# Kernel tuning notes

Measured on AMD Instinct MI355X. Metric: run time of the kernel, lower is better.

Reference implementation:

```python
import jax, jax.numpy as jnp
import numpy as np

B, IN, COND, HID, LAT, E = 8192, 512, 256, 1024, 128, 4
EPS = 1e-4  # RunningMeanStd epsilon

def leaky(x):
    return jax.nn.leaky_relu(x, 0.01)

def _norm(a, m, v):
    # RunningMeanStd.normalize: clip((a-mean)/sqrt(var+eps), -5, 5)
    return jnp.clip((a - m) / jnp.sqrt(v + EPS), -5.0, 5.0)

def setup_inputs() -> dict:
    key = jax.random.key(0)
    ks = iter(jax.random.split(key, 64))
    def rn(shape, scale=0.02):
        return jax.random.normal(next(ks), shape, dtype=jnp.float32) * scale
    z32 = lambda *s: jnp.zeros(s, jnp.float32)
    return {
        'x': rn((B, IN), 1.0), 'w': rn((B, COND), 1.0), 'eps': rn((B, LAT), 1.0),
        'rms_in_mean': z32(IN), 'rms_in_var': jnp.ones((IN,), jnp.float32),
        'rms_c_mean': z32(COND), 'rms_c_var': jnp.ones((COND,), jnp.float32),
        'enc_w0': rn((IN + COND, HID)), 'enc_b0': z32(HID),
        'enc_w1': rn((COND + HID, HID)), 'enc_b1': z32(HID),
        'enc_w2': rn((COND + HID, HID)), 'enc_b2': z32(HID),
        'enc_w3': rn((COND + HID, HID)), 'enc_b3': z32(HID),
        'mu_w': rn((HID, LAT)), 'mu_b': z32(LAT),
        'lv_w': rn((HID, LAT)), 'lv_b': z32(LAT),
        'g_w0': rn((LAT + COND, 64)), 'g_b0': z32(64),
        'g_w1': rn((64, 64)), 'g_b1': z32(64),
        'g_w2': rn((64, E)), 'g_b2': z32(E),
        'dec_w0': rn((E, LAT + COND, HID)), 'dec_b0': jnp.full((E, HID), 0.01, jnp.float32),
        'dec_w1': rn((E, LAT + COND + HID, HID)), 'dec_b1': jnp.full((E, HID), 0.01, jnp.float32),
        'dec_w2': rn((E, LAT + COND + HID, HID)), 'dec_b2': jnp.full((E, HID), 0.01, jnp.float32),
        'dec_w3': rn((E, LAT + COND + HID, HID)), 'dec_b3': jnp.full((E, HID), 0.01, jnp.float32),
        'dec_w4': rn((E, LAT + COND + HID, IN)), 'dec_b4': jnp.full((E, IN), 0.01, jnp.float32),
    }

def _forward(x, w, eps, rms_in_mean, rms_in_var, rms_c_mean, rms_c_var,
             enc_w0, enc_b0, enc_w1, enc_b1, enc_w2, enc_b2, enc_w3, enc_b3,
             mu_w, mu_b, lv_w, lv_b,
             g_w0, g_b0, g_w1, g_b1, g_w2, g_b2,
             dec_w0, dec_b0, dec_w1, dec_b1, dec_w2, dec_b2, dec_w3, dec_b3,
             dec_w4, dec_b4):
    xn = _norm(x, rms_in_mean, rms_in_var)
    wn = _norm(w, rms_c_mean, rms_c_var)
    wn = jnp.where(jnp.isnan(wn), 0.0, wn)
    # encoder: original encode() loop applies ONLY the Linear ops (LeakyReLUs skipped),
    # concatenating w before every Linear after the first
    h = jnp.concatenate([xn, wn], -1) @ enc_w0 + enc_b0
    for W, b in ((enc_w1, enc_b1), (enc_w2, enc_b2), (enc_w3, enc_b3)):
        h = jnp.concatenate([wn, h], -1) @ W + b
    mu = leaky(h) @ mu_w + mu_b
    log_var = jnp.clip(leaky(h) @ lv_w + lv_b, -5.0, 5.0)
    z = mu + eps * jnp.exp(0.5 * log_var)  # reparameterize
    # MixedDecoder: gate -> softmax coefficients over experts
    c = wn
    g = leaky(jnp.concatenate([z, c], -1) @ g_w0 + g_b0)
    g = leaky(g @ g_w1 + g_b1)
    coeff = jax.nn.softmax(g @ g_w2 + g_b2, axis=-1)  # [B, E]
    out = c
    layers = ((dec_w0, dec_b0, True), (dec_w1, dec_b1, True),
              (dec_w2, dec_b2, True), (dec_w3, dec_b3, True),
              (dec_w4, dec_b4, False))
    for i, (W, b, act) in enumerate(layers):
        inp = jnp.concatenate([z, out], -1) if i == 0 else jnp.concatenate([z, c, out], -1)
        # fused soft-MoE: sum_e coeff_e * (inp @ W_e) + coeff @ b_e
        he = jnp.einsum('bi,eio->beo', inp, W)          # [B, E, out_dim]
        o = jnp.einsum('beo,be->bo', he, coeff) + coeff @ b
        out = leaky(o) if act else o
    return z, out, mu, log_var

def reference(x, w, eps, rms_in_mean, rms_in_var, rms_c_mean, rms_c_var,
              enc_w0, enc_b0, enc_w1, enc_b1, enc_w2, enc_b2, enc_w3, enc_b3,
              mu_w, mu_b, lv_w, lv_b,
              g_w0, g_b0, g_w1, g_b1, g_w2, g_b2,
              dec_w0, dec_b0, dec_w1, dec_b1, dec_w2, dec_b2, dec_w3, dec_b3,
              dec_w4, dec_b4):
    return _forward(x, w, eps, rms_in_mean, rms_in_var, rms_c_mean, rms_c_var,
                    enc_w0, enc_b0, enc_w1, enc_b1, enc_w2, enc_b2, enc_w3, enc_b3,
                    mu_w, mu_b, lv_w, lv_b,
                    g_w0, g_b0, g_w1, g_b1, g_w2, g_b2,
                    dec_w0, dec_b0, dec_w1, dec_b1, dec_w2, dec_b2, dec_w3, dec_b3,
                    dec_w4, dec_b4)
```

## Files before the change

kernel.cpp:

```cpp
#include <hip/hip_runtime.h>

#define BATCH 8192

typedef __bf16 bf16x8 __attribute__((ext_vector_type(8)));
typedef float f32x4 __attribute__((ext_vector_type(4)));

__device__ __forceinline__ float leakyf(float x) { return x > 0.f ? x : 0.01f * x; }

__device__ __forceinline__ short f2bf(float f) {
    union { float f; unsigned u; } v; v.f = f;
    unsigned r = v.u + 0x7fffu + ((v.u >> 16) & 1u);
    return (short)(r >> 16);
}
__device__ __forceinline__ float bf2f(short s) {
    union { unsigned u; float f; } v; v.u = ((unsigned)(unsigned short)s) << 16;
    return v.f;
}

__global__ __launch_bounds__(256) void transconv_k(const float* __restrict__ in,
                                                   short* __restrict__ out,
                                                   int R, int C, int ldo) {
    __shared__ float t[32][33];
    const int r0 = blockIdx.y * 32, c0 = blockIdx.x * 32;
    const int tx = threadIdx.x, ty = threadIdx.y;
#pragma unroll
    for (int i = 0; i < 4; ++i)
        t[ty * 4 + i][tx] = in[(size_t)(r0 + ty * 4 + i) * C + c0 + tx];
    __syncthreads();
#pragma unroll
    for (int i = 0; i < 4; ++i)
        out[(size_t)(c0 + ty * 4 + i) * ldo + r0 + tx] = f2bf(t[tx][ty * 4 + i]);
}

__global__ __launch_bounds__(256) void transconv_moe_k(const float* __restrict__ in,
                                                       short* __restrict__ out, int C) {
    __shared__ float t[32][33];
    const int r0 = blockIdx.y * 32, c0 = blockIdx.x * 32;
    const int tx = threadIdx.x, ty = threadIdx.y;
#pragma unroll
    for (int i = 0; i < 4; ++i)
        t[ty * 4 + i][tx] = in[(size_t)(r0 + ty * 4 + i) * C + c0 + tx];
    __syncthreads();
    const int e = r0 / 1408, k = r0 - e * 1408;
    const int rp0 = (k < 384) ? (e * 384 + k) : (1536 + e * 1024 + (k - 384));
#pragma unroll
    for (int i = 0; i < 4; ++i)
        out[(size_t)(c0 + ty * 4 + i) * 5632 + rp0 + tx] = f2bf(t[tx][ty * 4 + i]);
}

template <int BM, int EPI>
__global__ __launch_bounds__(512) void mm_p3(
    const short* __restrict__ A, int lda,
    const short* __restrict__ Bt, int ldb,
    const float* __restrict__ bias, const float* __restrict__ coeff,
    short* __restrict__ Cb, float* __restrict__ Cf, int ldc, int N, int K) {
    constexpr int TSZA = BM * 64;
    constexpr int TSZB = 128 * 64;
    constexpr int RA = BM / 64;
    constexpr int WMR = BM / 4;
    constexpr int FM = WMR / 16;
    __shared__ short As[3 * TSZA];
    __shared__ short Bs[2 * TSZB];
    const int tid = threadIdx.x;
    const int wave = tid >> 6, lane = tid & 63;
    const int wm = wave >> 1, wq = wave & 1;

    int bx = blockIdx.x, by = blockIdx.y;
    {
        int nwg = gridDim.x * gridDim.y;
        if ((nwg & 7) == 0) {
            int flat = by * gridDim.x + bx;
            int nf = (flat & 7) * (nwg >> 3) + (flat >> 3);
            bx = nf % gridDim.x;
            by = nf / gridDim.x;
        }
    }
    const int m0 = by * BM, n0 = bx * 128;
    const int srow = lane >> 3;
    const int scolsw = ((lane & 7) ^ srow) << 3;
    const int l15 = lane & 15;
    const int khalf = (lane >> 4) << 3;

    auto stageA = [&](int kt, int buf) {
#pragma unroll
        for (int it = 0; it < RA; ++it) {
            int chunk = it * 8 + wave;
            int row = chunk * 8 + srow;
            const short* g = A + (size_t)(m0 + row) * lda + kt + scolsw;
            __builtin_amdgcn_global_load_lds(
                (const __attribute__((address_space(1))) void*)g,
                (__attribute__((address_space(3))) void*)(As + buf * TSZA + chunk * 512),
                16, 0, 0);
        }
    };
    auto stageB = [&](int kt, int buf) {
#pragma unroll
        for (int it = 0; it < 2; ++it) {
            int chunk = it * 8 + wave;
            int row = chunk * 8 + srow;
            const short* g = Bt + (size_t)(n0 + row) * ldb + kt + scolsw;
            __builtin_amdgcn_global_load_lds(
                (const __attribute__((address_space(1))) void*)g,
                (__attribute__((address_space(3))) void*)(Bs + buf * TSZB + chunk * 512),
                16, 0, 0);
        }
    };

    f32x4 acc[FM][4];
    const f32x4 z4 = {0.f, 0.f, 0.f, 0.f};
#pragma unroll
    for (int i = 0; i < FM; ++i)
#pragma unroll
        for (int j = 0; j < 4; ++j) acc[i][j] = z4;

    auto loadA = [&](const short* Ah, int kk, bf16x8 (&a)[FM]) {
#pragma unroll
        for (int i = 0; i < FM; ++i) {
            int R = wm * WMR + i * 16 + l15;
            a[i] = *(const bf16x8*)&Ah[R * 64 + ((kk * 32 + khalf) ^ ((R & 7) << 3))];
        }
    };
    auto loadB = [&](const short* Bh, int kk, bf16x8 (&b)[4]) {
#pragma unroll
        for (int j = 0; j < 4; ++j) {
            int R = wq * 64 + j * 16 + l15;
            b[j] = *(const bf16x8*)&Bh[R * 64 + ((kk * 32 + khalf) ^ ((R & 7) << 3))];
        }
    };
    auto domfma = [&](bf16x8 (&a)[FM], bf16x8 (&b)[4]) {
        __builtin_amdgcn_s_setprio(1);
#pragma unroll
        for (int i = 0; i < FM; ++i)
#pragma unroll
            for (int j = 0; j < 4; ++j)
                acc[i][j] = __builtin_amdgcn_mfma_f32_16x16x32_bf16(
                    a[i], b[j], acc[i][j], 0, 0, 0);
        __builtin_amdgcn_s_setprio(0);
    };

    const int nk = K >> 6;

    stageA(0, 0);
    stageB(0, 0);
    stageA(64, 1);
    __builtin_amdgcn_sched_barrier(0);
    if constexpr (BM == 256) {
        asm volatile("s_waitcnt vmcnt(4)" ::: "memory");
    } else {
        asm volatile("s_waitcnt vmcnt(2)" ::: "memory");
    }
    __builtin_amdgcn_s_barrier();
    __builtin_amdgcn_sched_barrier(0);

    bf16x8 a0[FM], b0[4], a1[FM], b1[4];
    loadA(As, 0, a0);
    loadB(Bs, 0, b0);

    int ia = 0;
    int is = 2;
#pragma unroll 1
    for (int t = 0; t < nk; ++t) {
        const short* Ah = As + ia * TSZA;
        const short* Bh = Bs + (t & 1) * TSZB;
        const int ian = (ia == 2) ? 0 : ia + 1;
        const short* Ah1 = As + ian * TSZA;
        const short* Bh1 = Bs + ((t + 1) & 1) * TSZB;

        loadA(Ah, 1, a1);
        loadB(Bh, 1, b1);
        if (t + 1 < nk) stageB((t + 1) << 6, (t + 1) & 1);
        __builtin_amdgcn_sched_barrier(0);
        __builtin_amdgcn_s_barrier();
        __builtin_amdgcn_sched_barrier(0);
        domfma(a0, b0);
        __builtin_amdgcn_sched_barrier(0);
        asm volatile("s_waitcnt vmcnt(0)" ::: "memory");
        __builtin_amdgcn_s_barrier();
        __builtin_amdgcn_sched_barrier(0);

        if (t + 1 < nk) {
            loadA(Ah1, 0, a0);
            loadB(Bh1, 0, b0);
        }
        if (t + 2 < nk) stageA((t + 2) << 6, is);
        __builtin_amdgcn_sched_barrier(0);
        __builtin_amdgcn_s_barrier();
        __builtin_amdgcn_sched_barrier(0);
        domfma(a1, b1);
        __builtin_amdgcn_sched_barrier(0);

        ia = ian;
        is = (is == 2) ? 0 : is + 1;
    }

#pragma unroll
    for (int i = 0; i < FM; ++i) {
#pragma unroll
        for (int r = 0; r < 4; ++r) {
            int row = m0 + wm * WMR + i * 16 + ((lane >> 4) << 2) + r;
#pragma unroll
            for (int j = 0; j < 4; ++j) {
                int col = n0 + wq * 64 + j * 16 + l15;
                float v = acc[i][j][r];
                if constexpr (EPI == 0) {
                    v += bias[col];
                    Cb[(size_t)row * ldc + col] = f2bf(v);
                } else if constexpr (EPI == 1) {
                    v = leakyf(v + bias[col]);
                    Cb[(size_t)row * ldc + col] = f2bf(v);
                } else if constexpr (EPI == 5) {
                    const float4 c4 = *reinterpret_cast<const float4*>(coeff + (size_t)row * 4);
                    v += c4.x * bias[col] + c4.y * bias[N + col] +
                         c4.z * bias[2 * N + col] + c4.w * bias[3 * N + col];
                    float a = leakyf(v);
                    Cb[(size_t)row * ldc + 0 * 1024 + col] = f2bf(c4.x * a);
                    Cb[(size_t)row * ldc + 1 * 1024 + col] = f2bf(c4.y * a);
                    Cb[(size_t)row * ldc + 2 * 1024 + col] = f2bf(c4.z * a);
                    Cb[(size_t)row * ldc + 3 * 1024 + col] = f2bf(c4.w * a);
                } else {
                    const float4 c4 = *reinterpret_cast<const float4*>(coeff + (size_t)row * 4);
                    v += c4.x * bias[col] + c4.y * bias[N + col] +
                         c4.z * bias[2 * N + col] + c4.w * bias[3 * N + col];
                    Cf[(size_t)row * ldc + col] = v;
                }
            }
        }
    }
}

template <int BM, int BN, int EPI>
__global__ __launch_bounds__(256) void mm_k(
    const short* __restrict__ A, int lda,
    const short* __restrict__ Bt, int ldb,
    const float* __restrict__ bias, const float* __restrict__ bias2,
    const float* __restrict__ coeff,
    short* __restrict__ Cb, float* __restrict__ Cf, float* __restrict__ Cf2,
    int ldc, int N, int K) {
    constexpr bool MOE = (EPI == 3 || EPI == 4);
    constexpr int WM = BM / 2, WN = BN / 2;
    constexpr int FM = WM / 16, FN = WN / 16;
    constexpr int ASZ = BM * 64, BSZ = BN * 64;
    __shared__ short As[2 * ASZ];
    __shared__ short Bs[2 * BSZ];
    const int tid = threadIdx.x;
    const int wave = tid >> 6, lane = tid & 63;
    const int wm = wave >> 1, wq = wave & 1;

    int bx = blockIdx.x, by = blockIdx.y;
    {
        int nwg = gridDim.x * gridDim.y;
        if ((nwg & 7) == 0) {
            int flat = by * gridDim.x + bx;
            int nf = (flat & 7) * (nwg >> 3) + (flat >> 3);
            bx = nf % gridDim.x;
            by = nf / gridDim.x;
        }
    }
    const int m0 = by * BM, n0 = bx * BN;
    const int srow = lane >> 3;
    const int scolsw = ((lane & 7) ^ srow) << 3;
    const int l15 = lane & 15;
    const int khalf = (lane >> 4) << 3;

    auto stage = [&](const short* Bsrc, int kt, int half) {
#pragma unroll
        for (int it = 0; it < BM / 32; ++it) {
            int chunk = it * 4 + wave;
            int row = chunk * 8 + srow;
            const short* g = A + (size_t)(m0 + row) * lda + kt + scolsw;
            __builtin_amdgcn_global_load_lds(
                (const __attribute__((address_space(1))) void*)g,
                (__attribute__((address_space(3))) void*)(As + half * ASZ + chunk * 512),
                16, 0, 0);
        }
#pragma unroll
        for (int it = 0; it < BN / 32; ++it) {
            int chunk = it * 4 + wave;
            int row = chunk * 8 + srow;
            const short* g = Bsrc + (size_t)(n0 + row) * ldb + kt + scolsw;
            __builtin_amdgcn_global_load_lds(
                (const __attribute__((address_space(1))) void*)g,
                (__attribute__((address_space(3))) void*)(Bs + half * BSZ + chunk * 512),
                16, 0, 0);
        }
    };

    f32x4 acc[FM][FN];
    f32x4 accf[MOE ? FM : 1][MOE ? FN : 1];
    const f32x4 z4 = {0.f, 0.f, 0.f, 0.f};
    if constexpr (MOE) {
#pragma unroll
        for (int i = 0; i < FM; ++i)
#pragma unroll
            for (int j = 0; j < FN; ++j) accf[i][j] = z4;
    }

    constexpr int NE = MOE ? 4 : 1;
    const int nk = K >> 6;
#pragma unroll 1
    for (int e = 0; e < NE; ++e) {
        const short* Be = Bt + (size_t)e * K;
#pragma unroll
        for (int i = 0; i < FM; ++i)
#pragma unroll
            for (int j = 0; j < FN; ++j) acc[i][j] = z4;

        stage(Be, 0, 0);
        __syncthreads();

#pragma unroll 1
        for (int t = 0; t < nk; ++t) {
            const int cur = t & 1;
            if (t + 1 < nk) stage(Be, (t + 1) << 6, cur ^ 1);
            const short* Ah = As + cur * ASZ;
            const short* Bh = Bs + cur * BSZ;
#pragma unroll
            for (int kk = 0; kk < 2; ++kk) {
                bf16x8 a[FM], b[FN];
#pragma unroll
                for (int i = 0; i < FM; ++i) {
                    int R = wm * WM + i * 16 + l15;
                    int off = (kk * 32 + khalf) ^ ((R & 7) << 3);
                    a[i] = *(const bf16x8*)&Ah[R * 64 + off];
                }
#pragma unroll
                for (int j = 0; j < FN; ++j) {
                    int R = wq * WN + j * 16 + l15;
                    int off = (kk * 32 + khalf) ^ ((R & 7) << 3);
                    b[j] = *(const bf16x8*)&Bh[R * 64 + off];
                }
#pragma unroll
                for (int i = 0; i < FM; ++i)
#pragma unroll
                    for (int j = 0; j < FN; ++j)
                        acc[i][j] = __builtin_amdgcn_mfma_f32_16x16x32_bf16(
                            a[i], b[j], acc[i][j], 0, 0, 0);
            }
            __syncthreads();
        }
        if constexpr (MOE) {
#pragma unroll
            for (int i = 0; i < FM; ++i) {
                int rbase = m0 + wm * WM + i * 16 + ((lane >> 4) << 2);
#pragma unroll
                for (int r = 0; r < 4; ++r) {
                    float ce = coeff[(size_t)(rbase + r) * 4 + e];
#pragma unroll
                    for (int j = 0; j < FN; ++j) accf[i][j][r] += ce * acc[i][j][r];
                }
            }
        }
    }

#pragma unroll
    for (int i = 0; i < FM; ++i) {
#pragma unroll
        for (int r = 0; r < 4; ++r) {
            int row = m0 + wm * WM + i * 16 + ((lane >> 4) << 2) + r;
#pragma unroll
            for (int j = 0; j < FN; ++j) {
                int col = n0 + wq * WN + j * 16 + l15;
                float v = MOE ? accf[i][j][r] : acc[i][j][r];
                if constexpr (EPI == 0) {
                    v += bias[col];
                    Cb[(size_t)row * ldc + col] = f2bf(v);
                } else if constexpr (EPI == 1) {
                    v = leakyf(v + bias[col]);
                    Cb[(size_t)row * ldc + col] = f2bf(v);
                } else if constexpr (EPI == 2) {
                    if (col < 128) {
                        Cf[(size_t)row * 128 + col] = v + bias[col];
                    } else {
                        float u = v + bias2[col - 128];
                        u = fminf(fmaxf(u, -5.f), 5.f);
                        Cf2[(size_t)row * 128 + (col - 128)] = u;
                    }
                } else if constexpr (EPI == 3) {
                    const float* c4 = coeff + (size_t)row * 4;
                    v += c4[0] * bias[col] + c4[1] * bias[N + col] +
                         c4[2] * bias[2 * N + col] + c4[3] * bias[3 * N + col];
                    Cb[(size_t)row * ldc + col] = f2bf(leakyf(v));
                } else {
                    const float* c4 = coeff + (size_t)row * 4;
                    v += c4[0] * bias[col] + c4[1] * bias[N + col] +
                         c4[2] * bias[2 * N + col] + c4[3] * bias[3 * N + col];
                    Cf[(size_t)row * ldc + col] = v;
                }
            }
        }
    }
}

__global__ __launch_bounds__(256) void norm_k(
    const float* __restrict__ x, const float* __restrict__ w,
    const float* __restrict__ im, const float* __restrict__ iv,
    const float* __restrict__ cm, const float* __restrict__ cv,
    short* __restrict__ enc0, short* __restrict__ encA,
    short* __restrict__ encB, short* __restrict__ dec0) {
    int idx = blockIdx.x * 256 + threadIdx.x;
    const int TX = BATCH * 512;
    if (idx < TX) {
        int b = idx >> 9, j = idx & 511;
        float v = (x[idx] - im[j]) * rsqrtf(iv[j] + 1e-4f);
        v = fminf(fmaxf(v, -5.f), 5.f);
        enc0[(size_t)b * 768 + j] = f2bf(v);
    } else {
        int k = idx - TX;
        if (k < BATCH * 256) {
            int b = k >> 8, j = k & 255;
            float v = (w[k] - cm[j]) * rsqrtf(cv[j] + 1e-4f);
            if (v != v) v = 0.f;
            v = fminf(fmaxf(v, -5.f), 5.f);
            short s = f2bf(v);
            enc0[(size_t)b * 768 + 512 + j] = s;
            encA[(size_t)b * 1280 + j] = s;
            encB[(size_t)b * 1280 + j] = s;
            dec0[(size_t)b * 384 + 128 + j] = s;
        }
    }
}

__global__ __launch_bounds__(256) void reparam_k(
    const float* __restrict__ mu, const float* __restrict__ lv,
    const float* __restrict__ eps, float* __restrict__ z, short* __restrict__ dec0) {
    int idx = blockIdx.x * 256 + threadIdx.x;
    if (idx >= BATCH * 128) return;
    float zv = mu[idx] + eps[idx] * expf(0.5f * lv[idx]);
    z[idx] = zv;
    int b = idx >> 7, j = idx & 127;
    dec0[(size_t)b * 384 + j] = f2bf(zv);
}

__global__ __launch_bounds__(256) void fill_zc_k(const short* __restrict__ dec0,
                                                 const float* __restrict__ cf,
                                                 short* __restrict__ dA,
                                                 short* __restrict__ dB) {
    int idx = blockIdx.x * 256 + threadIdx.x;
    if (idx >= BATCH * 1536) return;
    int b = idx / 1536, c = idx - b * 1536;
    int e = c / 384, k = c - e * 384;
    short s = f2bf(cf[(size_t)b * 4 + e] * bf2f(dec0[(size_t)b * 384 + k]));
    dA[(size_t)b * 5632 + c] = s;
    dB[(size_t)b * 5632 + c] = s;
}

__global__ __launch_bounds__(256) void fill_dec_k(const short* __restrict__ dec0,
                                                  short* __restrict__ decA,
                                                  short* __restrict__ decB) {
    int idx = blockIdx.x * 256 + threadIdx.x;
    if (idx >= BATCH * 384) return;
    int b = idx / 384, c = idx - b * 384;
    short s = dec0[idx];
    decA[(size_t)b * 1408 + c] = s;
    decB[(size_t)b * 1408 + c] = s;
}

__global__ __launch_bounds__(256) void gate_sm_k(const short* __restrict__ g1,
                                                 const float* __restrict__ w2,
                                                 const float* __restrict__ b2,
                                                 float* __restrict__ coeff) {
    int r = blockIdx.x * 256 + threadIdx.x;
    if (r >= BATCH) return;
    float l0 = b2[0], l1 = b2[1], l2 = b2[2], l3 = b2[3];
    const short* row = g1 + (size_t)r * 64;
#pragma unroll
    for (int k = 0; k < 64; ++k) {
        float gv = bf2f(row[k]);
        l0 += gv * w2[k * 4 + 0];
        l1 += gv * w2[k * 4 + 1];
        l2 += gv * w2[k * 4 + 2];
        l3 += gv * w2[k * 4 + 3];
    }
    float mx = fmaxf(fmaxf(l0, l1), fmaxf(l2, l3));
    float e0 = expf(l0 - mx), e1 = expf(l1 - mx), e2 = expf(l2 - mx), e3 = expf(l3 - mx);
    float s = 1.f / (e0 + e1 + e2 + e3);
    float4 outv = make_float4(e0 * s, e1 * s, e2 * s, e3 * s);
    *reinterpret_cast<float4*>(coeff + (size_t)r * 4) = outv;
}

extern "C" void kernel_launch(void* const* d_in, const int* in_sizes, int n_in,
                              void* d_out, int out_size, void* d_ws, size_t ws_size,
                              hipStream_t stream) {
    const float* x    = (const float*)d_in[0];
    const float* w    = (const float*)d_in[1];
    const float* epsv = (const float*)d_in[2];
    const float* rim  = (const float*)d_in[3];
    const float* riv  = (const float*)d_in[4];
    const float* rcm  = (const float*)d_in[5];
    const float* rcv  = (const float*)d_in[6];
    const float* ew0 = (const float*)d_in[7];  const float* eb0 = (const float*)d_in[8];
    const float* ew1 = (const float*)d_in[9];  const float* eb1 = (const float*)d_in[10];
    const float* ew2 = (const float*)d_in[11]; const float* eb2 = (const float*)d_in[12];
    const float* ew3 = (const float*)d_in[13]; const float* eb3 = (const float*)d_in[14];
    const float* muw = (const float*)d_in[15]; const float* mub = (const float*)d_in[16];
    const float* lvw = (const float*)d_in[17]; const float* lvb = (const float*)d_in[18];
    const float* gw0 = (const float*)d_in[19]; const float* gb0 = (const float*)d_in[20];
    const float* gw1 = (const float*)d_in[21]; const float* gb1 = (const float*)d_in[22];
    const float* gw2 = (const float*)d_in[23]; const float* gb2 = (const float*)d_in[24];
    const float* dw0 = (const float*)d_in[25]; const float* db0 = (const float*)d_in[26];
    const float* dw1 = (const float*)d_in[27]; const float* db1 = (const float*)d_in[28];
    const float* dw2 = (const float*)d_in[29]; const float* db2 = (const float*)d_in[30];
    const float* dw3 = (const float*)d_in[31]; const float* db3 = (const float*)d_in[32];
    const float* dw4 = (const float*)d_in[33]; const float* db4 = (const float*)d_in[34];

    float* out    = (float*)d_out;
    float* z_out  = out;
    float* y_out  = out + (size_t)BATCH * 128;
    float* mu_out = out + (size_t)BATCH * 640;
    float* lv_out = out + (size_t)BATCH * 768;

    char* cur = (char*)d_ws;
    auto alloc = [&](size_t bytes) -> char* {
        char* p = cur;
        cur += (bytes + 255) & ~(size_t)255;
        return p;
    };
    auto align256 = [](size_t b) { return (b + 255) & ~(size_t)255; };

    short* ew0t = (short*)alloc((size_t)768 * 1024 * 2);
    short* ew1t = (short*)alloc((size_t)1280 * 1024 * 2);
    short* ew2t = (short*)alloc((size_t)1280 * 1024 * 2);
    short* ew3t = (short*)alloc((size_t)1280 * 1024 * 2);
    short* hdWt = (short*)alloc((size_t)256 * 1024 * 2);
    short* gw0t = (short*)alloc((size_t)64 * 384 * 2);
    short* gw1t = (short*)alloc((size_t)64 * 64 * 2);
    short* dw0t = (short*)alloc((size_t)1024 * 1536 * 2);
    short* dw1t = (short*)alloc((size_t)1024 * 5632 * 2);
    short* dw2t = (short*)alloc((size_t)1024 * 5632 * 2);
    short* dw3t = (short*)alloc((size_t)1024 * 5632 * 2);
    short* dw4t = (short*)alloc((size_t)512 * 5632 * 2);
    short* dec0 = (short*)alloc((size_t)BATCH * 384 * 2);
    short* g0   = (short*)alloc((size_t)BATCH * 64 * 2);
    short* g1   = (short*)alloc((size_t)BATCH * 64 * 2);
    float* cf   = (float*)alloc((size_t)BATCH * 4 * 4);

    char* region = cur;
    const size_t bigA = align256((size_t)BATCH * 5632 * 2);
    const size_t fastNeed = (size_t)(region - (char*)d_ws) + 2 * bigA;
    const bool fast = (ws_size >= fastNeed);

    short* enc0 = (short*)region;
    short* encA = (short*)(region + align256((size_t)BATCH * 768 * 2));
    short* encB = (short*)((char*)encA + align256((size_t)BATCH * 1280 * 2));
    short* hl   = encB;
    short* dAp = (short*)region;
    short* dBp = (short*)(region + bigA);
    short* decA = (short*)region;
    short* decB = (short*)(region + align256((size_t)BATCH * 1408 * 2));

    dim3 blk(256);
    dim3 blk5(512);
    dim3 tblk(32, 8);

    transconv_k<<<dim3(1024 / 32, 768 / 32), tblk, 0, stream>>>(ew0, ew0t, 768, 1024, 768);
    transconv_k<<<dim3(1024 / 32, 1280 / 32), tblk, 0, stream>>>(ew1, ew1t, 1280, 1024, 1280);
    transconv_k<<<dim3(1024 / 32, 1280 / 32), tblk, 0, stream>>>(ew2, ew2t, 1280, 1024, 1280);
    transconv_k<<<dim3(1024 / 32, 1280 / 32), tblk, 0, stream>>>(ew3, ew3t, 1280, 1024, 1280);
    transconv_k<<<dim3(128 / 32, 1024 / 32), tblk, 0, stream>>>(muw, hdWt, 1024, 128, 1024);
    transconv_k<<<dim3(128 / 32, 1024 / 32), tblk, 0, stream>>>(lvw, hdWt + (size_t)128 * 1024, 1024, 128, 1024);
    transconv_k<<<dim3(64 / 32, 384 / 32), tblk, 0, stream>>>(gw0, gw0t, 384, 64, 384);
    transconv_k<<<dim3(64 / 32, 64 / 32), tblk, 0, stream>>>(gw1, gw1t, 64, 64, 64);
    transconv_k<<<dim3(1024 / 32, 1536 / 32), tblk, 0, stream>>>(dw0, dw0t, 1536, 1024, 1536);
    if (fast) {
        transconv_moe_k<<<dim3(1024 / 32, 5632 / 32), tblk, 0, stream>>>(dw1, dw1t, 1024);
        transconv_moe_k<<<dim3(1024 / 32, 5632 / 32), tblk, 0, stream>>>(dw2, dw2t, 1024);
        transconv_moe_k<<<dim3(1024 / 32, 5632 / 32), tblk, 0, stream>>>(dw3, dw3t, 1024);
        transconv_moe_k<<<dim3(512 / 32, 5632 / 32), tblk, 0, stream>>>(dw4, dw4t, 512);
    } else {
        transconv_k<<<dim3(1024 / 32, 5632 / 32), tblk, 0, stream>>>(dw1, dw1t, 5632, 1024, 5632);
        transconv_k<<<dim3(1024 / 32, 5632 / 32), tblk, 0, stream>>>(dw2, dw2t, 5632, 1024, 5632);
        transconv_k<<<dim3(1024 / 32, 5632 / 32), tblk, 0, stream>>>(dw3, dw3t, 5632, 1024, 5632);
        transconv_k<<<dim3(512 / 32, 5632 / 32), tblk, 0, stream>>>(dw4, dw4t, 5632, 512, 5632);
    }

    norm_k<<<dim3(BATCH * 768 / 256), blk, 0, stream>>>(x, w, rim, riv, rcm, rcv,
                                                        enc0, encA, encB, dec0);

    dim3 gBig(1024 / 128, BATCH / 256);
    mm_p3<256, 0><<<gBig, blk5, 0, stream>>>(enc0, 768, ew0t, 768, eb0, nullptr,
                                             encA + 256, nullptr, 1280, 1024, 768);
    mm_p3<256, 0><<<gBig, blk5, 0, stream>>>(encA, 1280, ew1t, 1280, eb1, nullptr,
                                             encB + 256, nullptr, 1280, 1024, 1280);
    mm_p3<256, 0><<<gBig, blk5, 0, stream>>>(encB, 1280, ew2t, 1280, eb2, nullptr,
                                             encA + 256, nullptr, 1280, 1024, 1280);
    mm_p3<256, 1><<<gBig, blk5, 0, stream>>>(encA, 1280, ew3t, 1280, eb3, nullptr,
                                             hl, nullptr, 1024, 1024, 1280);

    mm_k<64, 128, 2><<<dim3(2, BATCH / 64), blk, 0, stream>>>(hl, 1024, hdWt, 1024, mub, lvb,
                                                              nullptr, nullptr, mu_out, lv_out,
                                                              0, 256, 1024);

    reparam_k<<<dim3(BATCH * 128 / 256), blk, 0, stream>>>(mu_out, lv_out, epsv, z_out, dec0);

    mm_k<64, 64, 1><<<dim3(1, BATCH / 64), blk, 0, stream>>>(dec0, 384, gw0t, 384, gb0, nullptr,
                                                             nullptr, g0, nullptr, nullptr,
                                                             64, 64, 384);
    mm_k<64, 64, 1><<<dim3(1, BATCH / 64), blk, 0, stream>>>(g0, 64, gw1t, 64, gb1, nullptr,
                                                             nullptr, g1, nullptr, nullptr,
                                                             64, 64, 64);
    gate_sm_k<<<dim3(BATCH / 256), blk, 0, stream>>>(g1, gw2, gb2, cf);

    if (fast) {
        fill_zc_k<<<dim3(BATCH * 1536 / 256), blk, 0, stream>>>(dec0, cf, dAp, dBp);
        mm_p3<256, 5><<<gBig, blk5, 0, stream>>>(dAp, 5632, dw0t, 1536, db0, cf,
                                                 dAp + 1536, nullptr, 5632, 1024, 1536);
        mm_p3<256, 5><<<gBig, blk5, 0, stream>>>(dAp, 5632, dw1t, 5632, db1, cf,
                                                 dBp + 1536, nullptr, 5632, 1024, 5632);
        mm_p3<256, 5><<<gBig, blk5, 0, stream>>>(dBp, 5632, dw2t, 5632, db2, cf,
                                                 dAp + 1536, nullptr, 5632, 1024, 5632);
        mm_p3<256, 5><<<gBig, blk5, 0, stream>>>(dAp, 5632, dw3t, 5632, db3, cf,
                                                 dBp + 1536, nullptr, 5632, 1024, 5632);
        mm_p3<128, 6><<<dim3(512 / 128, BATCH / 128), blk5, 0, stream>>>(
            dBp, 5632, dw4t, 5632, db4, cf, nullptr, y_out, 512, 512, 5632);
    } else {
        fill_dec_k<<<dim3(BATCH * 384 / 256), blk, 0, stream>>>(dec0, decA, decB);
        dim3 gDec(1024 / 128, BATCH / 128);
        mm_k<128, 128, 3><<<gDec, blk, 0, stream>>>(dec0, 384, dw0t, 1536, db0, nullptr, cf,
                                                    decA + 384, nullptr, nullptr, 1408, 1024, 384);
        mm_k<128, 128, 3><<<gDec, blk, 0, stream>>>(decA, 1408, dw1t, 5632, db1, nullptr, cf,
                                                    decB + 384, nullptr, nullptr, 1408, 1024, 1408);
        mm_k<128, 128, 3><<<gDec, blk, 0, stream>>>(decB, 1408, dw2t, 5632, db2, nullptr, cf,
                                                    decA + 384, nullptr, nullptr, 1408, 1024, 1408);
        mm_k<128, 128, 3><<<gDec, blk, 0, stream>>>(decA, 1408, dw3t, 5632, db3, nullptr, cf,
                                                    decB + 384, nullptr, nullptr, 1408, 1024, 1408);
        mm_k<128, 128, 4><<<dim3(512 / 128, BATCH / 128), blk, 0, stream>>>(
            decB, 1408, dw4t, 5632, db4, nullptr, cf, nullptr, y_out, nullptr, 512, 512, 1408);
    }
}
```

Measured before the change: 718.0 us.

## Restructure GEMM main loop to drop register double-buffering of LDS fragments

Replaces the register ping-pong scheme, where the next half-tile fragments were loaded from LDS while the current MFMAs ran, with a simpler loop. Each half-k step now loads its fragments and immediately issues its MFMAs. The vmcnt wait is relaxed to keep the in-flight A prefetch outstanding, and there is one fewer barrier per half-step. This cuts register pressure and barrier count, but LDS read latency is no longer hidden behind MFMAs within a wave.

```diff
diff --git a/kernel.cpp b/kernel.cpp
--- a/kernel.cpp
+++ b/kernel.cpp
@@ -105,6 +105,13 @@
                 16, 0, 0);
         }
     };
+    auto waitRA = [&]() {
+        if constexpr (BM == 256) {
+            asm volatile("s_waitcnt vmcnt(4)" ::: "memory");
+        } else {
+            asm volatile("s_waitcnt vmcnt(2)" ::: "memory");
+        }
+    };
 
     f32x4 acc[FM][4];
     const f32x4 z4 = {0.f, 0.f, 0.f, 0.f};
@@ -112,31 +119,6 @@
     for (int i = 0; i < FM; ++i)
 #pragma unroll
         for (int j = 0; j < 4; ++j) acc[i][j] = z4;
-
-    auto loadA = [&](const short* Ah, int kk, bf16x8 (&a)[FM]) {
-#pragma unroll
-        for (int i = 0; i < FM; ++i) {
-            int R = wm * WMR + i * 16 + l15;
-            a[i] = *(const bf16x8*)&Ah[R * 64 + ((kk * 32 + khalf) ^ ((R & 7) << 3))];
-        }
-    };
-    auto loadB = [&](const short* Bh, int kk, bf16x8 (&b)[4]) {
-#pragma unroll
-        for (int j = 0; j < 4; ++j) {
-            int R = wq * 64 + j * 16 + l15;
-            b[j] = *(const bf16x8*)&Bh[R * 64 + ((kk * 32 + khalf) ^ ((R & 7) << 3))];
-        }
-    };
-    auto domfma = [&](bf16x8 (&a)[FM], bf16x8 (&b)[4]) {
-        __builtin_amdgcn_s_setprio(1);
-#pragma unroll
-        for (int i = 0; i < FM; ++i)
-#pragma unroll
-            for (int j = 0; j < 4; ++j)
-                acc[i][j] = __builtin_amdgcn_mfma_f32_16x16x32_bf16(
-                    a[i], b[j], acc[i][j], 0, 0, 0);
-        __builtin_amdgcn_s_setprio(0);
-    };
 
     const int nk = K >> 6;
 
@@ -144,17 +126,9 @@
     stageB(0, 0);
     stageA(64, 1);
     __builtin_amdgcn_sched_barrier(0);
-    if constexpr (BM == 256) {
-        asm volatile("s_waitcnt vmcnt(4)" ::: "memory");
-    } else {
-        asm volatile("s_waitcnt vmcnt(2)" ::: "memory");
-    }
+    waitRA();
     __builtin_amdgcn_s_barrier();
     __builtin_amdgcn_sched_barrier(0);
-
-    bf16x8 a0[FM], b0[4], a1[FM], b1[4];
-    loadA(As, 0, a0);
-    loadB(Bs, 0, b0);
 
     int ia = 0;
     int is = 2;
@@ -162,34 +136,66 @@
     for (int t = 0; t < nk; ++t) {
         const short* Ah = As + ia * TSZA;
         const short* Bh = Bs + (t & 1) * TSZB;
-        const int ian = (ia == 2) ? 0 : ia + 1;
-        const short* Ah1 = As + ian * TSZA;
-        const short* Bh1 = Bs + ((t + 1) & 1) * TSZB;
-
-        loadA(Ah, 1, a1);
-        loadB(Bh, 1, b1);
-        if (t + 1 < nk) stageB((t + 1) << 6, (t + 1) & 1);
-        __builtin_amdgcn_sched_barrier(0);
-        __builtin_amdgcn_s_barrier();
-        __builtin_amdgcn_sched_barrier(0);
-        domfma(a0, b0);
-        __builtin_amdgcn_sched_barrier(0);
-        asm volatile("s_waitcnt vmcnt(0)" ::: "memory");
-        __builtin_amdgcn_s_barrier();
-        __builtin_amdgcn_sched_barrier(0);
-
-        if (t + 1 < nk) {
-            loadA(Ah1, 0, a0);
-            loadB(Bh1, 0, b0);
-        }
-        if (t + 2 < nk) stageA((t + 2) << 6, is);
-        __builtin_amdgcn_sched_barrier(0);
-        __builtin_amdgcn_s_barrier();
-        __builtin_amdgcn_sched_barrier(0);
-        domfma(a1, b1);
-        __builtin_amdgcn_sched_barrier(0);
-
-        ia = ian;
+
+        {
+            bf16x8 a[FM], b[4];
+#pragma unroll
+            for (int i = 0; i < FM; ++i) {
+                int R = wm * WMR + i * 16 + l15;
+                a[i] = *(const bf16x8*)&Ah[R * 64 + (khalf ^ ((R & 7) << 3))];
+            }
+#pragma unroll
+            for (int j = 0; j < 4; ++j) {
+                int R = wq * 64 + j * 16 + l15;
+                b[j] = *(const bf16x8*)&Bh[R * 64 + (khalf ^ ((R & 7) << 3))];
+            }
+            if (t + 1 < nk) stageB((t + 1) << 6, (t + 1) & 1);
+            __builtin_amdgcn_sched_barrier(0);
+            __builtin_amdgcn_s_setprio(1);
+#pragma unroll
+            for (int i = 0; i < FM; ++i)
+#pragma unroll
+                for (int j = 0; j < 4; ++j)
+                    acc[i][j] = __builtin_amdgcn_mfma_f32_16x16x32_bf16(
+                        a[i], b[j], acc[i][j], 0, 0, 0);
+            __builtin_amdgcn_s_setprio(0);
+            __builtin_amdgcn_sched_barrier(0);
+            __builtin_amdgcn_s_barrier();
+        }
+
+        {
+            bf16x8 a[FM], b[4];
+#pragma unroll
+            for (int i = 0; i < FM; ++i) {
+                int R = wm * WMR + i * 16 + l15;
+                a[i] = *(const bf16x8*)&Ah[R * 64 + ((32 + khalf) ^ ((R & 7) << 3))];
+            }
+#pragma unroll
+            for (int j = 0; j < 4; ++j) {
+                int R = wq * 64 + j * 16 + l15;
+                b[j] = *(const bf16x8*)&Bh[R * 64 + ((32 + khalf) ^ ((R & 7) << 3))];
+            }
+            if (t + 2 < nk) stageA((t + 2) << 6, is);
+            __builtin_amdgcn_sched_barrier(0);
+            __builtin_amdgcn_s_setprio(1);
+#pragma unroll
+            for (int i = 0; i < FM; ++i)
+#pragma unroll
+                for (int j = 0; j < 4; ++j)
+                    acc[i][j] = __builtin_amdgcn_mfma_f32_16x16x32_bf16(
+                        a[i], b[j], acc[i][j], 0, 0, 0);
+            __builtin_amdgcn_s_setprio(0);
+            __builtin_amdgcn_sched_barrier(0);
+            if (t + 1 < nk) {
+                if (t + 2 < nk) {
+                    waitRA();
+                } else {
+                    asm volatile("s_waitcnt vmcnt(0)" ::: "memory");
+                }
+            }
+            __builtin_amdgcn_s_barrier();
+        }
+        ia = (ia == 2) ? 0 : ia + 1;
         is = (is == 2) ? 0 : is + 1;
     }
 
```

Result: no change. 715.1 us (-0.4%).
